# Kernel optimization log

Measured on AMD Instinct MI355X. Metric: run time of the kernel, lower is better.

## Reference

```python
import jax, jax.numpy as jnp
import numpy as np

B, N1, N2 = 4, 16384, 4096   # scenes, fine points/scene, coarse points/scene
CIN, COUT = 512, 256
K = 3
EPS_BN = 1e-5
EPS_D = 1e-8


def setup_inputs() -> dict:
    key = jax.random.key(0)
    ks = jax.random.split(key, 6)
    return {
        "point_1": jax.random.uniform(ks[0], (B * N1, 3), dtype=jnp.float32),
        "feat_1": jax.random.normal(ks[1], (B * N1, COUT), dtype=jnp.float32) * 0.1,
        "point_2": jax.random.uniform(ks[2], (B * N2, 3), dtype=jnp.float32),
        "feat_2": jax.random.normal(ks[3], (B * N2, CIN), dtype=jnp.float32) * 0.1,
        "W1": jax.random.normal(ks[4], (COUT, COUT), dtype=jnp.float32) / np.sqrt(COUT).astype(np.float32),
        "b1": jnp.zeros((COUT,), jnp.float32),
        "g1": jnp.ones((COUT,), jnp.float32),
        "beta1": jnp.zeros((COUT,), jnp.float32),
        "W2": jax.random.normal(ks[5], (CIN, COUT), dtype=jnp.float32) / np.sqrt(CIN).astype(np.float32),
        "b2": jnp.zeros((COUT,), jnp.float32),
        "g2": jnp.ones((COUT,), jnp.float32),
        "beta2": jnp.zeros((COUT,), jnp.float32),
        # equal-sized segments: row_splits = [0, N, 2N, ...]
        "row_splits_1": jnp.arange(B + 1, dtype=jnp.int32) * N1,
        "row_splits_2": jnp.arange(B + 1, dtype=jnp.int32) * N2,
    }


def _bn(x, gamma, beta):
    # BatchNorm1d, training mode (biased variance, as in torch)
    mu = x.mean(0)
    var = x.var(0)
    return gamma * (x - mu) * jax.lax.rsqrt(var + EPS_BN) + beta


def reference(point_1, feat_1, point_2, feat_2,
              W1, b1, g1, beta1, W2, b2, g2, beta2,
              row_splits_1, row_splits_2):
    # linear1(feat_1): Linear + BN + ReLU
    f1 = jax.nn.relu(_bn(feat_1 @ W1 + b1, g1, beta1))          # [B*N1, COUT]
    # linear2(feat_2): Linear + BN + ReLU
    f2 = jax.nn.relu(_bn(feat_2 @ W2 + b2, g2, beta2))          # [B*N2, COUT]

    # batched KNN (equal row_splits -> reshape into [B, n, 3])
    q = point_1.reshape(B, N1, 3)
    p = point_2.reshape(B, N2, 3)
    d2 = ((q * q).sum(-1)[:, :, None]
          + (p * p).sum(-1)[:, None, :]
          - 2.0 * jnp.einsum("bnd,bmd->bnm", q, p))             # [B, N1, N2] squared dists
    neg_d, idx = jax.lax.top_k(-d2, K)                           # [B, N1, K]
    dist = jnp.maximum(-neg_d, 0.0)

    # inverse-distance weights (knn search is non-differentiable in the original)
    recip = 1.0 / (dist + EPS_D)
    w = jax.lax.stop_gradient(recip / recip.sum(-1, keepdims=True))  # [B, N1, K]

    # gather + weighted sum (three-interpolate)
    f2b = f2.reshape(B, N2, COUT)
    gathered = f2b[jnp.arange(B)[:, None, None], idx]            # [B, N1, K, COUT]
    interp = (gathered * w[..., None]).sum(2).reshape(B * N1, COUT)

    return f1 + interp
```

## Files before the change

kernel.cpp:

```cpp
#include <hip/hip_runtime.h>
#include <hip/hip_bf16.h>
#include <math.h>

#define N1R 65536
#define N2R 16384
#define NPB 4096
#define NQB 16384
#define CC  256
#define ASTRIDE 40
#define NCELL 512
#define GRID_FAIL_R2 0.015625f

typedef __attribute__((ext_vector_type(4))) float v4f;
typedef __attribute__((ext_vector_type(8))) short v8s;

static __device__ __forceinline__ short f2bs(float f) {
    union { __hip_bfloat16 h; short s; } u;
    u.h = __float2bfloat16(f);
    return u.s;
}

static __device__ __forceinline__ int cell_of(float x, float y, float z) {
    const int cx = min(7, (int)(x * 8.0f));
    const int cy = min(7, (int)(y * 8.0f));
    const int cz = min(7, (int)(z * 8.0f));
    return (cz << 6) | (cy << 3) | cx;
}

static __device__ __forceinline__ void ins3(float d, int si,
    float& b0, float& b1, float& b2, int& i0, int& i1, int& i2)
{
    const bool lt0 = (d < b0) | ((d == b0) & (si < i0));
    const bool lt1 = (d < b1) | ((d == b1) & (si < i1));
    const bool lt2 = (d < b2) | ((d == b2) & (si < i2));
    b2 = lt1 ? b1 : (lt2 ? d : b2);   i2 = lt1 ? i1 : (lt2 ? si : i2);
    b1 = lt0 ? b0 : (lt1 ? d : b1);   i1 = lt0 ? i0 : (lt1 ? si : i1);
    b0 = lt0 ? d  : b0;               i0 = lt0 ? si : i0;
}

__global__ __launch_bounds__(256)
void wtrans_all_kernel(const float* __restrict__ W1f, const float* __restrict__ W2f,
                       short* __restrict__ WT1, short* __restrict__ WT2)
{
    const int i = blockIdx.x * 256 + threadIdx.x;
    if (i < 65536) {
        const int k = i >> 8, n = i & 255;
        WT1[(size_t)n * 256 + k] = f2bs(W1f[i]);
    } else {
        const int j = i - 65536;
        const int k = j >> 8, n = j & 255;
        WT2[(size_t)n * 512 + k] = f2bs(W2f[j]);
    }
}

__global__ __launch_bounds__(256)
void hist_kernel(const float* __restrict__ p2, const float* __restrict__ p1,
                 float4* __restrict__ paug,
                 int* __restrict__ counts_p, int* __restrict__ counts_q)
{
#pragma clang fp contract(off)
    if (blockIdx.x < 64) {
        const int i = blockIdx.x * 256 + threadIdx.x;
        const float x = p2[(size_t)i * 3 + 0];
        const float y = p2[(size_t)i * 3 + 1];
        const float z = p2[(size_t)i * 3 + 2];
        float4 v;
        v.x = x; v.y = y; v.z = z;
        v.w = (x * x + y * y) + z * z;
        paug[i] = v;
        const int b = i >> 12;
        atomicAdd(&counts_p[b * NCELL + cell_of(x, y, z)], 1);
    } else {
        const int i = (blockIdx.x - 64) * 256 + threadIdx.x;
        const float x = p1[(size_t)i * 3 + 0];
        const float y = p1[(size_t)i * 3 + 1];
        const float z = p1[(size_t)i * 3 + 2];
        const int b = i >> 14;
        atomicAdd(&counts_q[b * NCELL + cell_of(x, y, z)], 1);
    }
}

__global__ __launch_bounds__(512)
void prefix_kernel(const int* __restrict__ counts_p, int* __restrict__ cursors_p,
                   int* __restrict__ starts_p,
                   const int* __restrict__ counts_q, int* __restrict__ cursors_q)
{
    __shared__ int sc[512];
    const int t = threadIdx.x;
    for (int a = 0; a < 8; ++a) {
        const int b = a & 3;
        const int* cnt = (a < 4) ? counts_p + b * NCELL : counts_q + b * NCELL;
        const int v = cnt[t];
        sc[t] = v;
        __syncthreads();
        for (int off = 1; off < 512; off <<= 1) {
            const int add = (t >= off) ? sc[t - off] : 0;
            __syncthreads();
            sc[t] += add;
            __syncthreads();
        }
        const int incl = sc[t];
        const int excl = incl - v;
        if (a < 4) {
            starts_p[b * 513 + t] = excl;
            if (t == 511) starts_p[b * 513 + 512] = incl;
            cursors_p[b * NCELL + t] = excl;
        } else {
            cursors_q[b * NCELL + t] = excl;
        }
        __syncthreads();
    }
}

__global__ __launch_bounds__(256)
void scatter_kernel(const float4* __restrict__ paug, const float* __restrict__ p1,
                    int* __restrict__ cursors_p, int* __restrict__ cursors_q,
                    float4* __restrict__ sortedP, unsigned short* __restrict__ sIdx,
                    unsigned short* __restrict__ qlist)
{
    if (blockIdx.x < 64) {
        const int i = blockIdx.x * 256 + threadIdx.x;
        const float4 v = paug[i];
        const int b = i >> 12;
        const int cell = cell_of(v.x, v.y, v.z);
        const int pos = atomicAdd(&cursors_p[b * NCELL + cell], 1);
        sortedP[(size_t)b * NPB + pos] = v;
        sIdx[(size_t)b * NPB + pos] = (unsigned short)(i & 4095);
    } else {
        const int i = (blockIdx.x - 64) * 256 + threadIdx.x;
        const float x = p1[(size_t)i * 3 + 0];
        const float y = p1[(size_t)i * 3 + 1];
        const float z = p1[(size_t)i * 3 + 2];
        const int b = i >> 14;
        const int cell = cell_of(x, y, z);
        const int pos = atomicAdd(&cursors_q[b * NCELL + cell], 1);
        qlist[(size_t)b * NQB + pos] = (unsigned short)(i & 16383);
    }
}

template<int BM>
__global__ __launch_bounds__(256)
void gemm_fused_kernel(const float* __restrict__ X,
                       const short* __restrict__ WT,
                       const float* __restrict__ bias,
                       float* __restrict__ Y,
                       float* __restrict__ partS, float* __restrict__ partQ,
                       int Kdim)
{
    __shared__ short As[2][BM * ASTRIDE];

    constexpr int MI  = BM / 32;
    constexpr int NPF = BM / 32;
    constexpr int TPR = 256 / BM;
    constexpr int FPT = BM / 8;

    const int bm0 = blockIdx.x * BM;
    const int bn0 = blockIdx.y * 128;
    const int wave = threadIdx.x >> 6;
    const int lane = threadIdx.x & 63;
    const int wm0 = (wave >> 1) * (BM / 2);
    const int wn0 = (wave & 1) * 64;
    const int col = lane & 15, quad = lane >> 4;

    const int srow = threadIdx.x / TPR;
    const int skh  = (threadIdx.x % TPR) * FPT;
    const float* sbase = X + (size_t)(bm0 + srow) * Kdim + skh;
    short* sdst0 = &As[0][srow * ASTRIDE + skh];
    short* sdst1 = &As[1][srow * ASTRIDE + skh];

    v4f acc[MI][4];
#pragma unroll
    for (int i = 0; i < MI; ++i)
#pragma unroll
        for (int j = 0; j < 4; ++j) acc[i][j] = (v4f){0.f, 0.f, 0.f, 0.f};

    const short* wbase = WT + (size_t)(bn0 + wn0 + col) * Kdim + quad * 8;

    v4f pf[NPF];
#pragma unroll
    for (int i = 0; i < NPF; ++i) pf[i] = *(const v4f*)(sbase + i * 4);
    {
        v8s wv;
#pragma unroll
        for (int j = 0; j < NPF / 2; ++j) {
#pragma unroll
            for (int t = 0; t < 4; ++t) {
                wv[t]     = f2bs(pf[2 * j][t]);
                wv[t + 4] = f2bs(pf[2 * j + 1][t]);
            }
            *(v8s*)(sdst0 + j * 8) = wv;
        }
    }
    if (32 < Kdim)
#pragma unroll
        for (int i = 0; i < NPF; ++i) pf[i] = *(const v4f*)(sbase + 32 + i * 4);

    const int NC = Kdim >> 5;
    for (int c = 0; c < NC; ++c) {
        const int k0 = c << 5;
        const bool more = (c + 1 < NC);

        v8s wv[NPF / 2];
        if (more) {
#pragma unroll
            for (int j = 0; j < NPF / 2; ++j)
#pragma unroll
                for (int t = 0; t < 4; ++t) {
                    wv[j][t]     = f2bs(pf[2 * j][t]);
                    wv[j][t + 4] = f2bs(pf[2 * j + 1][t]);
                }
        }
        __syncthreads();
        if (more) {
            short* sd = (c & 1) ? sdst0 : sdst1;
#pragma unroll
            for (int j = 0; j < NPF / 2; ++j) *(v8s*)(sd + j * 8) = wv[j];
        }

        v8s bf[4];
#pragma unroll
        for (int ni = 0; ni < 4; ++ni)
            bf[ni] = *(const v8s*)(wbase + (size_t)(ni * 16) * Kdim + k0);

        if (c + 2 < NC) {
            const float* np = sbase + k0 + 64;
#pragma unroll
            for (int i = 0; i < NPF; ++i) pf[i] = *(const v4f*)(np + i * 4);
        }

        const short* bufc = As[c & 1];
        v8s a[MI];
#pragma unroll
        for (int mi = 0; mi < MI; ++mi)
            a[mi] = *(const v8s*)(bufc + (wm0 + mi * 16 + col) * ASTRIDE + quad * 8);
#pragma unroll
        for (int mi = 0; mi < MI; ++mi)
#pragma unroll
            for (int ni = 0; ni < 4; ++ni)
                acc[mi][ni] = __builtin_amdgcn_mfma_f32_16x16x32_bf16(a[mi], bf[ni], acc[mi][ni], 0, 0, 0);
    }

    float* pS = partS + (size_t)(blockIdx.x * 2 + (wave >> 1)) * CC;
    float* pQ = partQ + (size_t)(blockIdx.x * 2 + (wave >> 1)) * CC;
#pragma unroll
    for (int ni = 0; ni < 4; ++ni) {
        const int n = bn0 + wn0 + ni * 16 + col;
        const float bv = bias[n];
        float s = 0.f, q = 0.f;
#pragma unroll
        for (int mi = 0; mi < MI; ++mi) {
            const int m = bm0 + wm0 + mi * 16 + quad * 4;
#pragma unroll
            for (int r = 0; r < 4; ++r) {
                const float y = acc[mi][ni][r] + bv;
                Y[(size_t)(m + r) * CC + n] = y;
                s += y; q += y * y;
            }
        }
        s += __shfl_xor(s, 16); q += __shfl_xor(q, 16);
        s += __shfl_xor(s, 32); q += __shfl_xor(q, 32);
        if (quad == 0) { pS[n] = s; pQ[n] = q; }
    }
}

__global__ __launch_bounds__(256)
void stat_reduce_kernel(const float* __restrict__ pS1, const float* __restrict__ pQ1,
                        const float* __restrict__ pS2, const float* __restrict__ pQ2,
                        float* __restrict__ stats)
{
    const int c = threadIdx.x;
    const bool two = blockIdx.x >= 16;
    const float* pS = two ? pS2 : pS1;
    const float* pQ = two ? pQ2 : pQ1;
    const int r0 = (two ? (blockIdx.x - 16) : blockIdx.x) * 64;
    float s = 0.f, q = 0.f;
    for (int r = r0; r < r0 + 64; ++r) {
        s += pS[(size_t)r * CC + c];
        q += pQ[(size_t)r * CC + c];
    }
    float* st = stats + (two ? 512 : 0);
    atomicAdd(&st[c], s);
    atomicAdd(&st[256 + c], q);
}

__global__ __launch_bounds__(512)
void finalize_kernel(const float* __restrict__ sums,
                     const float* __restrict__ g1, const float* __restrict__ be1,
                     const float* __restrict__ g2, const float* __restrict__ be2,
                     float* __restrict__ ac)
{
    const int t = threadIdx.x;
    const int c = t & 255;
    const int which = t >> 8;
    const float* s = sums + which * 512;
    const double n = which ? (double)N2R : (double)N1R;
    const double mu = (double)s[c] / n;
    const double var = (double)s[c + 256] / n - mu * mu;
    const float g  = which ? g2[c]  : g1[c];
    const float be = which ? be2[c] : be1[c];
    const double a  = (double)g / sqrt(var + 1e-5);
    const double cv = (double)be - a * mu;
    ac[which * 512 + c]       = (float)a;
    ac[which * 512 + 256 + c] = (float)cv;
}

__global__ __launch_bounds__(256)
void knn_grid_kernel(const float* __restrict__ p1,
                     const float4* __restrict__ sortedP,
                     const unsigned short* __restrict__ sIdx16,
                     const int* __restrict__ starts_p,
                     const unsigned short* __restrict__ qlist,
                     int* __restrict__ idx_out, float* __restrict__ w_out,
                     int* __restrict__ failCount, int* __restrict__ failList)
{
#pragma clang fp contract(off)
    __shared__ float4 sP[NPB];
    __shared__ unsigned short sI[NPB];
    __shared__ int sS[513];
    __shared__ float mD[128 * 3];
    __shared__ int   mI[128 * 3];

    const int b = blockIdx.x >> 7;
    const int slot0 = (blockIdx.x & 127) * 128;
    const int tid = threadIdx.x;
    const int lq = tid & 127;
    const int half = tid >> 7;

    {
        const float4* gp = sortedP + (size_t)b * NPB;
        for (int i = tid; i < NPB; i += 256) sP[i] = gp[i];
        const unsigned int* gi = (const unsigned int*)(sIdx16 + (size_t)b * NPB);
        unsigned int* li = (unsigned int*)sI;
        for (int i = tid; i < NPB / 2; i += 256) li[i] = gi[i];
        const int* gs = starts_p + b * 513;
        for (int i = tid; i < 513; i += 256) sS[i] = gs[i];
    }

    const int q = qlist[(size_t)b * NQB + slot0 + lq];
    const int qid = b * NQB + q;
    const float qx = p1[(size_t)qid * 3 + 0];
    const float qy = p1[(size_t)qid * 3 + 1];
    const float qz = p1[(size_t)qid * 3 + 2];
    const float qq = (qx * qx + qy * qy) + qz * qz;
    const int cqx = min(7, (int)(qx * 8.0f));
    const int cqy = min(7, (int)(qy * 8.0f));
    const int cqz = min(7, (int)(qz * 8.0f));

    __syncthreads();

    float b0 = 3.0e38f, b1 = 3.0e38f, b2 = 3.0e38f;
    int i0 = 0x7fffffff, i1 = 0x7fffffff, i2 = 0x7fffffff;

    int n = 0;
    for (int dz = -1; dz <= 1; ++dz)
        for (int dy = -1; dy <= 1; ++dy)
            for (int dx = -1; dx <= 1; ++dx, ++n) {
                if (half ? (n < 14) : (n >= 14)) continue;
                const int cz = cqz + dz, cy = cqy + dy, cx = cqx + dx;
                if (((unsigned)cz | (unsigned)cy | (unsigned)cx) > 7u) continue;
                const int cell = (cz << 6) | (cy << 3) | cx;
                const int ks = sS[cell], ke = sS[cell + 1];
                for (int k = ks; k < ke; ++k) {
                    const float4 P = sP[k];
                    const int si = sI[k];
                    const float dot = fmaf(qz, P.z, fmaf(qy, P.y, qx * P.x));
                    const float d = fmaf(-2.0f, dot, qq + P.w);
                    ins3(d, si, b0, b1, b2, i0, i1, i2);
                }
            }

    if (half) {
        mD[lq * 3 + 0] = b0; mD[lq * 3 + 1] = b1; mD[lq * 3 + 2] = b2;
        mI[lq * 3 + 0] = i0; mI[lq * 3 + 1] = i1; mI[lq * 3 + 2] = i2;
    }
    __syncthreads();
    if (!half) {
#pragma unroll
        for (int r = 0; r < 3; ++r)
            ins3(mD[lq * 3 + r], mI[lq * 3 + r], b0, b1, b2, i0, i1, i2);

        if (!(b2 < GRID_FAIL_R2)) {
            const int p = atomicAdd(failCount, 1);
            if (p < N1R) failList[p] = qid;
        }
        const float r0 = 1.0f / (fmaxf(b0, 0.0f) + 1e-8f);
        const float r1 = 1.0f / (fmaxf(b1, 0.0f) + 1e-8f);
        const float r2 = 1.0f / (fmaxf(b2, 0.0f) + 1e-8f);
        const float rs = (r0 + r1) + r2;
        idx_out[(size_t)qid * 3 + 0] = i0;
        idx_out[(size_t)qid * 3 + 1] = i1;
        idx_out[(size_t)qid * 3 + 2] = i2;
        w_out[(size_t)qid * 3 + 0] = r0 / rs;
        w_out[(size_t)qid * 3 + 1] = r1 / rs;
        w_out[(size_t)qid * 3 + 2] = r2 / rs;
    }
}

__global__ __launch_bounds__(256)
void knn_bf_kernel(const float* __restrict__ p1,
                   const float4* __restrict__ paug,
                   const int* __restrict__ failCount,
                   const int* __restrict__ failList,
                   int* __restrict__ idx_out, float* __restrict__ w_out)
{
#pragma clang fp contract(off)
    const int nf = min(*failCount, N1R);
    const int gw = (blockIdx.x * 256 + threadIdx.x) >> 6;
    const int lane = threadIdx.x & 63;
    const int nw = (gridDim.x * 256) >> 6;

    for (int fi = gw; fi < nf; fi += nw) {
        const int qid = failList[fi];
        const int b = qid >> 14;
        const float qx = p1[(size_t)qid * 3 + 0];
        const float qy = p1[(size_t)qid * 3 + 1];
        const float qz = p1[(size_t)qid * 3 + 2];
        const float qq = (qx * qx + qy * qy) + qz * qz;

        float b0 = 3.0e38f, b1 = 3.0e38f, b2 = 3.0e38f;
        int i0 = 0x7fffffff, i1 = 0x7fffffff, i2 = 0x7fffffff;

        const float4* pb = paug + (size_t)b * NPB;
        for (int j = lane; j < NPB; j += 64) {
            const float4 P = pb[j];
            const float dot = fmaf(qz, P.z, fmaf(qy, P.y, qx * P.x));
            const float d = fmaf(-2.0f, dot, qq + P.w);
            ins3(d, j, b0, b1, b2, i0, i1, i2);
        }
        for (int m = 1; m < 64; m <<= 1) {
            const float c0 = __shfl_xor(b0, m), c1 = __shfl_xor(b1, m), c2 = __shfl_xor(b2, m);
            const int j0 = __shfl_xor(i0, m), j1 = __shfl_xor(i1, m), j2 = __shfl_xor(i2, m);
            ins3(c0, j0, b0, b1, b2, i0, i1, i2);
            ins3(c1, j1, b0, b1, b2, i0, i1, i2);
            ins3(c2, j2, b0, b1, b2, i0, i1, i2);
        }
        if (lane == 0) {
            const float r0 = 1.0f / (fmaxf(b0, 0.0f) + 1e-8f);
            const float r1 = 1.0f / (fmaxf(b1, 0.0f) + 1e-8f);
            const float r2 = 1.0f / (fmaxf(b2, 0.0f) + 1e-8f);
            const float rs = (r0 + r1) + r2;
            idx_out[(size_t)qid * 3 + 0] = i0;
            idx_out[(size_t)qid * 3 + 1] = i1;
            idx_out[(size_t)qid * 3 + 2] = i2;
            w_out[(size_t)qid * 3 + 0] = r0 / rs;
            w_out[(size_t)qid * 3 + 1] = r1 / rs;
            w_out[(size_t)qid * 3 + 2] = r2 / rs;
        }
    }
}

__global__ __launch_bounds__(256)
void final_kernel(float* __restrict__ Y1out,
                  const float* __restrict__ Y2raw,
                  const float* __restrict__ ac,
                  const int* __restrict__ idx, const float* __restrict__ w,
                  const unsigned short* __restrict__ qlist)
{
    const int slot = blockIdx.x * 4 + (threadIdx.x >> 6);
    const int b = slot >> 14;
    const int r = b * NQB + qlist[slot];
    const int cg = threadIdx.x & 63;

    v4f a1 = *(const v4f*)(ac + cg * 4);
    v4f c1 = *(const v4f*)(ac + 256 + cg * 4);
    v4f a2 = *(const v4f*)(ac + 512 + cg * 4);
    v4f c2 = *(const v4f*)(ac + 768 + cg * 4);
    v4f y = *(const v4f*)(Y1out + (size_t)r * CC + cg * 4);
    v4f s;
#pragma unroll
    for (int j = 0; j < 4; ++j)
        s[j] = fmaxf(fmaf(a1[j], y[j], c1[j]), 0.f);

    const int*   ir = idx + (size_t)r * 3;
    const float* wr = w   + (size_t)r * 3;
#pragma unroll
    for (int k = 0; k < 3; ++k) {
        const int id = ir[k];
        const float wk = wr[k];
        v4f g = *(const v4f*)(Y2raw + ((size_t)(b * NPB + id)) * CC + cg * 4);
#pragma unroll
        for (int j = 0; j < 4; ++j) {
            const float gv = fmaxf(fmaf(a2[j], g[j], c2[j]), 0.f);
            s[j] = fmaf(wk, gv, s[j]);
        }
    }
    *(v4f*)(Y1out + (size_t)r * CC + cg * 4) = s;
}

extern "C" void kernel_launch(void* const* d_in, const int* in_sizes, int n_in,
                              void* d_out, int out_size, void* d_ws, size_t ws_size,
                              hipStream_t stream)
{
    const float* point1 = (const float*)d_in[0];
    const float* feat1  = (const float*)d_in[1];
    const float* point2 = (const float*)d_in[2];
    const float* feat2  = (const float*)d_in[3];
    const float* W1     = (const float*)d_in[4];
    const float* b1     = (const float*)d_in[5];
    const float* g1     = (const float*)d_in[6];
    const float* beta1  = (const float*)d_in[7];
    const float* W2     = (const float*)d_in[8];
    const float* b2     = (const float*)d_in[9];
    const float* g2     = (const float*)d_in[10];
    const float* beta2  = (const float*)d_in[11];

    float* Y1 = (float*)d_out;

    char* ws = (char*)d_ws;
    float*          Y2       = (float*)ws;
    float*          stats    = (float*)(ws + (size_t)16777216);
    int*            counts_p = (int*)  (ws + (size_t)16781312);
    int*            counts_q = (int*)  (ws + (size_t)16789504);
    int*            failCnt  = (int*)  (ws + (size_t)16797696);
    int*            cursors_p= (int*)  (ws + (size_t)16801792);
    int*            cursors_q= (int*)  (ws + (size_t)16809984);
    int*            starts_p = (int*)  (ws + (size_t)16818176);
    float*          ac       = (float*)(ws + (size_t)16826624);
    unsigned short* sIdx16   = (unsigned short*)(ws + (size_t)16830720);
    unsigned short* qlist    = (unsigned short*)(ws + (size_t)16863488);
    int*            failList = (int*)  (ws + (size_t)16994560);
    float4*         sortedP  = (float4*)(ws + (size_t)17256704);
    int*            idxb     = (int*)  (ws + (size_t)17518848);
    float*          wb       = (float*)(ws + (size_t)18305280);
    short*          WT1      = (short*)(ws + (size_t)19091712);
    short*          WT2      = (short*)(ws + (size_t)19222784);
    float4*         paug     = (float4*)(ws + (size_t)19484928);
    float*          partS1   = (float*)(ws + (size_t)19747072);
    float*          partQ1   = (float*)(ws + (size_t)20795648);
    float*          partS2   = (float*)(ws + (size_t)21844224);
    float*          partQ2   = (float*)(ws + (size_t)22368512);

    hipMemsetAsync(stats, 0, 24576, stream);

    wtrans_all_kernel<<<768, 256, 0, stream>>>(W1, W2, WT1, WT2);
    hist_kernel<<<320, 256, 0, stream>>>(point2, point1, paug, counts_p, counts_q);
    prefix_kernel<<<1, 512, 0, stream>>>(counts_p, cursors_p, starts_p, counts_q, cursors_q);
    scatter_kernel<<<320, 256, 0, stream>>>(paug, point1, cursors_p, cursors_q,
                                            sortedP, sIdx16, qlist);

    gemm_fused_kernel<128><<<dim3(N1R / 128, 2), 256, 0, stream>>>(feat1, WT1, b1, Y1,
                                                                   partS1, partQ1, 256);
    gemm_fused_kernel<64><<<dim3(N2R / 64, 2), 256, 0, stream>>>(feat2, WT2, b2, Y2,
                                                                 partS2, partQ2, 512);

    stat_reduce_kernel<<<24, 256, 0, stream>>>(partS1, partQ1, partS2, partQ2, stats);
    finalize_kernel<<<1, 512, 0, stream>>>(stats, g1, beta1, g2, beta2, ac);

    knn_grid_kernel<<<512, 256, 0, stream>>>(point1, sortedP, sIdx16, starts_p,
                                             qlist, idxb, wb, failCnt, failList);
    knn_bf_kernel<<<256, 256, 0, stream>>>(point1, paug, failCnt, failList, idxb, wb);

    final_kernel<<<N1R / 4, 256, 0, stream>>>(Y1, Y2, ac, idxb, wb, qlist);
}
```

Before: 315.4 us.

## Merge prep and GEMM launches, use wave-shuffle scan in prefix kernel

Fuses the weight-transpose and histogram kernels into one launch, and the two GEMM launches into one grid that dispatches on block id to the BM=128 or BM=64 path with a shared LDS buffer. The prefix scan moves from a 512-thread LDS Hillis-Steele scan with many barriers to a wave-level shuffle scan plus a small cross-wave combine. The aim is fewer kernel launches and less idle tail between dependent stages. The BM=64 blocks now allocate the larger 128-row LDS buffer, which may lower their occupancy.

```diff
diff --git a/kernel.cpp b/kernel.cpp
--- a/kernel.cpp
+++ b/kernel.cpp
@@ -39,28 +39,26 @@
 }
 
 __global__ __launch_bounds__(256)
-void wtrans_all_kernel(const float* __restrict__ W1f, const float* __restrict__ W2f,
-                       short* __restrict__ WT1, short* __restrict__ WT2)
-{
-    const int i = blockIdx.x * 256 + threadIdx.x;
-    if (i < 65536) {
-        const int k = i >> 8, n = i & 255;
-        WT1[(size_t)n * 256 + k] = f2bs(W1f[i]);
-    } else {
-        const int j = i - 65536;
-        const int k = j >> 8, n = j & 255;
-        WT2[(size_t)n * 512 + k] = f2bs(W2f[j]);
-    }
-}
-
-__global__ __launch_bounds__(256)
-void hist_kernel(const float* __restrict__ p2, const float* __restrict__ p1,
+void prep_kernel(const float* __restrict__ W1f, const float* __restrict__ W2f,
+                 short* __restrict__ WT1, short* __restrict__ WT2,
+                 const float* __restrict__ p2, const float* __restrict__ p1,
                  float4* __restrict__ paug,
                  int* __restrict__ counts_p, int* __restrict__ counts_q)
 {
 #pragma clang fp contract(off)
-    if (blockIdx.x < 64) {
-        const int i = blockIdx.x * 256 + threadIdx.x;
+    const int bid = blockIdx.x;
+    if (bid < 768) {
+        const int i = bid * 256 + threadIdx.x;
+        if (i < 65536) {
+            const int k = i >> 8, n = i & 255;
+            WT1[(size_t)n * 256 + k] = f2bs(W1f[i]);
+        } else {
+            const int j = i - 65536;
+            const int k = j >> 8, n = j & 255;
+            WT2[(size_t)n * 512 + k] = f2bs(W2f[j]);
+        }
+    } else if (bid < 832) {
+        const int i = (bid - 768) * 256 + threadIdx.x;
         const float x = p2[(size_t)i * 3 + 0];
         const float y = p2[(size_t)i * 3 + 1];
         const float z = p2[(size_t)i * 3 + 2];
@@ -71,7 +69,7 @@
         const int b = i >> 12;
         atomicAdd(&counts_p[b * NCELL + cell_of(x, y, z)], 1);
     } else {
-        const int i = (blockIdx.x - 64) * 256 + threadIdx.x;
+        const int i = (bid - 832) * 256 + threadIdx.x;
         const float x = p1[(size_t)i * 3 + 0];
         const float y = p1[(size_t)i * 3 + 1];
         const float z = p1[(size_t)i * 3 + 2];
@@ -85,25 +83,33 @@
                    int* __restrict__ starts_p,
                    const int* __restrict__ counts_q, int* __restrict__ cursors_q)
 {
-    __shared__ int sc[512];
+    __shared__ int sw[8];
+    __shared__ int sbase[8];
     const int t = threadIdx.x;
+    const int lane = t & 63, wid = t >> 6;
     for (int a = 0; a < 8; ++a) {
         const int b = a & 3;
         const int* cnt = (a < 4) ? counts_p + b * NCELL : counts_q + b * NCELL;
         const int v = cnt[t];
-        sc[t] = v;
+        int incl = v;
+#pragma unroll
+        for (int off = 1; off < 64; off <<= 1) {
+            const int u = __shfl_up(incl, off);
+            incl += (lane >= off) ? u : 0;
+        }
+        if (lane == 63) sw[wid] = incl;
         __syncthreads();
-        for (int off = 1; off < 512; off <<= 1) {
-            const int add = (t >= off) ? sc[t - off] : 0;
-            __syncthreads();
-            sc[t] += add;
-            __syncthreads();
-        }
-        const int incl = sc[t];
-        const int excl = incl - v;
+        if (t == 0) {
+            int s = 0;
+#pragma unroll
+            for (int w = 0; w < 8; ++w) { const int x = sw[w]; sbase[w] = s; s += x; }
+        }
+        __syncthreads();
+        const int inclT = incl + sbase[wid];
+        const int excl = inclT - v;
         if (a < 4) {
             starts_p[b * 513 + t] = excl;
-            if (t == 511) starts_p[b * 513 + 512] = incl;
+            if (t == 511) starts_p[b * 513 + 512] = inclT;
             cursors_p[b * NCELL + t] = excl;
         } else {
             cursors_q[b * NCELL + t] = excl;
@@ -139,23 +145,20 @@
 }
 
 template<int BM>
-__global__ __launch_bounds__(256)
-void gemm_fused_kernel(const float* __restrict__ X,
-                       const short* __restrict__ WT,
-                       const float* __restrict__ bias,
-                       float* __restrict__ Y,
-                       float* __restrict__ partS, float* __restrict__ partQ,
-                       int Kdim)
-{
-    __shared__ short As[2][BM * ASTRIDE];
-
+static __device__ __forceinline__ void gemm_body(
+    int bx, int by,
+    const float* __restrict__ X, const short* __restrict__ WT,
+    const float* __restrict__ bias, float* __restrict__ Y,
+    float* __restrict__ partS, float* __restrict__ partQ,
+    int Kdim, short* __restrict__ As0, short* __restrict__ As1)
+{
     constexpr int MI  = BM / 32;
     constexpr int NPF = BM / 32;
     constexpr int TPR = 256 / BM;
     constexpr int FPT = BM / 8;
 
-    const int bm0 = blockIdx.x * BM;
-    const int bn0 = blockIdx.y * 128;
+    const int bm0 = bx * BM;
+    const int bn0 = by * 128;
     const int wave = threadIdx.x >> 6;
     const int lane = threadIdx.x & 63;
     const int wm0 = (wave >> 1) * (BM / 2);
@@ -165,8 +168,8 @@
     const int srow = threadIdx.x / TPR;
     const int skh  = (threadIdx.x % TPR) * FPT;
     const float* sbase = X + (size_t)(bm0 + srow) * Kdim + skh;
-    short* sdst0 = &As[0][srow * ASTRIDE + skh];
-    short* sdst1 = &As[1][srow * ASTRIDE + skh];
+    short* sdst0 = As0 + srow * ASTRIDE + skh;
+    short* sdst1 = As1 + srow * ASTRIDE + skh;
 
     v4f acc[MI][4];
 #pragma unroll
@@ -228,7 +231,7 @@
             for (int i = 0; i < NPF; ++i) pf[i] = *(const v4f*)(np + i * 4);
         }
 
-        const short* bufc = As[c & 1];
+        const short* bufc = (c & 1) ? As1 : As0;
         v8s a[MI];
 #pragma unroll
         for (int mi = 0; mi < MI; ++mi)
@@ -240,8 +243,8 @@
                 acc[mi][ni] = __builtin_amdgcn_mfma_f32_16x16x32_bf16(a[mi], bf[ni], acc[mi][ni], 0, 0, 0);
     }
 
-    float* pS = partS + (size_t)(blockIdx.x * 2 + (wave >> 1)) * CC;
-    float* pQ = partQ + (size_t)(blockIdx.x * 2 + (wave >> 1)) * CC;
+    float* pS = partS + (size_t)(bx * 2 + (wave >> 1)) * CC;
+    float* pQ = partQ + (size_t)(bx * 2 + (wave >> 1)) * CC;
 #pragma unroll
     for (int ni = 0; ni < 4; ++ni) {
         const int n = bn0 + wn0 + ni * 16 + col;
@@ -260,6 +263,26 @@
         s += __shfl_xor(s, 16); q += __shfl_xor(q, 16);
         s += __shfl_xor(s, 32); q += __shfl_xor(q, 32);
         if (quad == 0) { pS[n] = s; pQ[n] = q; }
+    }
+}
+
+__global__ __launch_bounds__(256)
+void gemm_both_kernel(const float* __restrict__ feat1, const short* __restrict__ WT1,
+                      const float* __restrict__ b1, float* __restrict__ Y1,
+                      float* __restrict__ pS1, float* __restrict__ pQ1,
+                      const float* __restrict__ feat2, const short* __restrict__ WT2,
+                      const float* __restrict__ b2, float* __restrict__ Y2,
+                      float* __restrict__ pS2, float* __restrict__ pQ2)
+{
+    __shared__ short As[2][128 * ASTRIDE];
+    const int id = blockIdx.x;
+    if (id < 1024) {
+        gemm_body<128>(id >> 1, id & 1, feat1, WT1, b1, Y1, pS1, pQ1, 256,
+                       As[0], As[1]);
+    } else {
+        const int j = id - 1024;
+        gemm_body<64>(j >> 1, j & 1, feat2, WT2, b2, Y2, pS2, pQ2, 512,
+                      As[0], As[1]);
     }
 }
 
@@ -532,16 +555,14 @@
 
     hipMemsetAsync(stats, 0, 24576, stream);
 
-    wtrans_all_kernel<<<768, 256, 0, stream>>>(W1, W2, WT1, WT2);
-    hist_kernel<<<320, 256, 0, stream>>>(point2, point1, paug, counts_p, counts_q);
+    prep_kernel<<<1088, 256, 0, stream>>>(W1, W2, WT1, WT2, point2, point1,
+                                          paug, counts_p, counts_q);
     prefix_kernel<<<1, 512, 0, stream>>>(counts_p, cursors_p, starts_p, counts_q, cursors_q);
     scatter_kernel<<<320, 256, 0, stream>>>(paug, point1, cursors_p, cursors_q,
                                             sortedP, sIdx16, qlist);
 
-    gemm_fused_kernel<128><<<dim3(N1R / 128, 2), 256, 0, stream>>>(feat1, WT1, b1, Y1,
-                                                                   partS1, partQ1, 256);
-    gemm_fused_kernel<64><<<dim3(N2R / 64, 2), 256, 0, stream>>>(feat2, WT2, b2, Y2,
-                                                                 partS2, partQ2, 512);
+    gemm_both_kernel<<<1536, 256, 0, stream>>>(feat1, WT1, b1, Y1, partS1, partQ1,
+                                               feat2, WT2, b2, Y2, partS2, partQ2);
 
     stat_reduce_kernel<<<24, 256, 0, stream>>>(partS1, partQ1, partS2, partQ2, stats);
     finalize_kernel<<<1, 512, 0, stream>>>(stats, g1, beta1, g2, beta2, ac);
```

Result: faster. 306.0 us (-3.0%).
